# Performance work log

Measured on AMD Instinct MI355X. Metric: run time of the kernel, lower is better.

Reference implementation:

```python
import jax, jax.numpy as jnp
import numpy as np

B, H, S, D = 2, 16, 2048, 64

def setup_inputs() -> dict:
    key = jax.random.key(0)
    kq, kk, kv, km = jax.random.split(key, 4)
    Q = jax.random.normal(kq, (B, H, S, D), dtype=jnp.float32)
    K = jax.random.normal(kk, (B, H, S, D), dtype=jnp.float32)
    V = jax.random.normal(kv, (B, H, S, D), dtype=jnp.float32)
    attn_mask = jax.random.bernoulli(km, 0.5, (B, H, S, S))  # True = masked
    return {"Q": Q, "K": K, "V": V, "attn_mask": attn_mask}

def reference(Q, K, V, attn_mask):
    eps = 1e-12
    d_tensor = K.shape[-1]
    # scores: [B, H, S, S]
    scores = jnp.einsum('bhqd,bhkd->bhqk', Q, K) / np.sqrt(d_tensor).astype(jnp.float32)
    # Faithful to source: first fill mask==0 positions with -eps, then mask==True with -1e9.
    scores = jnp.where(attn_mask == 0, jnp.float32(-eps), scores)
    scores = jnp.where(attn_mask, jnp.float32(-1e9), scores)
    attn = jax.nn.softmax(scores, axis=-1)
    context = jnp.einsum('bhqk,bhkd->bhqd', attn, V)
    # dropout=0.0 (eval) -> identity
    return (context, attn)
```

## Files before the change

### kernel.cpp

```cpp
#include <hip/hip_runtime.h>
#include <hip/hip_bf16.h>
#include <stdint.h>

#define S 2048
#define D 64
#define BH 32
#define NROWS (BH * S)
#define CTX_ELEMS (NROWS * D)
#define NVTB 512
#define NSTB 2048
#define VT_BYTES ((size_t)BH * 64 * 64 * 32 * 2)

typedef __attribute__((ext_vector_type(8))) __bf16 bf16x8;
typedef __attribute__((ext_vector_type(4))) float f32x4;
typedef __attribute__((ext_vector_type(4))) int   i32x4;


__global__ __launch_bounds__(256) void k_mask(const int* __restrict__ mask,
                                              const float* __restrict__ V,
                                              float* __restrict__ attn,
                                              uint32_t* __restrict__ packed,
                                              __bf16* __restrict__ VT,
                                              int use_vt) {
  const int t = threadIdx.x;

  if (blockIdx.x < NVTB) {
    if (!use_vt) return;
    const int bh = blockIdx.x >> 4;
    const int kk0 = (blockIdx.x & 15) * 4;
    const int c = t >> 2;
    const int g = t & 3;
#pragma unroll
    for (int s = 0; s < 4; ++s) {
      const int kk = kk0 + s;
      const float* vp = V + ((long)bh * S + kk * 32 + g * 8) * D + c;
      bf16x8 o;
#pragma unroll
      for (int j = 0; j < 8; ++j) o[j] = (__bf16)vp[(long)j * D];
      *reinterpret_cast<bf16x8*>(VT + (((long)bh * 64 + kk) * 64 + c) * 32 + g * 8) = o;
    }
    return;
  }

  const int lane = t & 63;
  const int W = (blockIdx.x - NVTB) * 4 + (t >> 6);

#pragma unroll 1
  for (int row = W; row < NROWS; row += NSTB * 4) {
    const int* mrow = mask + (long)row * S;

    uint32_t nib = 0;
#pragma unroll
    for (int j = 0; j < 8; ++j) {
      const i32x4 m = __builtin_nontemporal_load(
          (const i32x4*)(mrow + j * 256 + lane * 4));
      nib |= (m[0] == 0 ? 1u : 0u) << (j * 4);
      nib |= (m[1] == 0 ? 1u : 0u) << (j * 4 + 1);
      nib |= (m[2] == 0 ? 1u : 0u) << (j * 4 + 2);
      nib |= (m[3] == 0 ? 1u : 0u) << (j * 4 + 3);
    }

    int cnt = __popc(nib);
#pragma unroll
    for (int off = 1; off < 64; off <<= 1) cnt += __shfl_xor(cnt, off, 64);
    const float inv = (cnt > 0) ? (1.0f / (float)cnt) : 0.0f;

    float* arow = attn + (long)row * S;
#pragma unroll
    for (int j = 0; j < 8; ++j) {
      f32x4 a;
      a[0] = ((nib >> (j * 4)) & 1u)     ? inv : 0.0f;
      a[1] = ((nib >> (j * 4 + 1)) & 1u) ? inv : 0.0f;
      a[2] = ((nib >> (j * 4 + 2)) & 1u) ? inv : 0.0f;
      a[3] = ((nib >> (j * 4 + 3)) & 1u) ? inv : 0.0f;
      __builtin_nontemporal_store(a, (f32x4*)(arow + j * 256 + lane * 4));
    }

    uint32_t word = 0;
    const int jsel = 4 * (lane >> 3);
    const int lbase = (lane & 7) * 8;
#pragma unroll
    for (int d = 0; d < 8; ++d) {
      const uint32_t nw = (uint32_t)__shfl((int)nib, lbase + d, 64);
      word |= ((nw >> jsel) & 0xFu) << (4 * d);
    }
    packed[(long)row * 64 + lane] = word;
  }
}

#define BMC 64
template<bool USE_VT>
__global__ __launch_bounds__(128) void k_ctx(const uint32_t* __restrict__ packed,
                                             const float* __restrict__ V,
                                             const __bf16* __restrict__ VT,
                                             float* __restrict__ ctx) {
  const int flat = blockIdx.x;
  const int wid = (flat & 7) * ((NROWS / BMC) / 8) + (flat >> 3);
  const int qt = wid & 31;
  const int bh = wid >> 5;

  const int t = threadIdx.x;
  const int lane = t & 63;
  const int w = t >> 6;
  const int l15 = lane & 15;
  const int lk = lane >> 4;

  __shared__ uint32_t pk[BMC * 65];
  __shared__ float invs[BMC];

  const long R0 = (long)bh * S + (long)qt * BMC;

  for (int i = t; i < BMC * 64; i += 128)
    pk[(i >> 6) * 65 + (i & 63)] = packed[(R0 + (i >> 6)) * 64 + (i & 63)];
  __syncthreads();

  if (t < BMC) {
    int c = 0;
#pragma unroll
    for (int i = 0; i < 64; ++i) c += __popc(pk[t * 65 + i]);
    invs[t] = (c > 0) ? (1.0f / (float)c) : 0.0f;
  }
  __syncthreads();

  const uint8_t* pkb = (const uint8_t*)pk;
  const uint8_t* ap[2];
#pragma unroll
  for (int mt = 0; mt < 2; ++mt)
    ap[mt] = pkb + (w * 32 + mt * 16 + l15) * 260 + lk;
  const __bf16* vt0 = VT + ((long)bh * 64) * 64 * 32 + (long)l15 * 32 + lk * 8;
  const float* vf0 = V + (long)bh * S * D + (long)lk * 8 * D + l15;

  f32x4 acc[2][4];
#pragma unroll
  for (int a = 0; a < 2; ++a)
#pragma unroll
    for (int b = 0; b < 4; ++b) acc[a][b] = f32x4{0.f, 0.f, 0.f, 0.f};

  auto LOADB = [&](bf16x8* dst, uint32_t* by, int kk) {
    if (USE_VT) {
#pragma unroll
      for (int n4 = 0; n4 < 4; ++n4)
        dst[n4] = *reinterpret_cast<const bf16x8*>(vt0 + ((long)kk * 64 + n4 * 16) * 32);
    } else {
      const float* vp = vf0 + (long)kk * 32 * D;
#pragma unroll
      for (int n4 = 0; n4 < 4; ++n4) {
        bf16x8 x;
#pragma unroll
        for (int j = 0; j < 8; ++j) x[j] = (__bf16)vp[j * D + n4 * 16];
        dst[n4] = x;
      }
    }
#pragma unroll
    for (int mt = 0; mt < 2; ++mt) by[mt] = ap[mt][kk * 4];
  };

  auto COMPUTE = [&](const bf16x8* bf, const uint32_t* by) {
#pragma unroll
    for (int mt = 0; mt < 2; ++mt) {
      union { uint32_t u[4]; bf16x8 v; } am;
#pragma unroll
      for (int p = 0; p < 4; ++p) {
        am.u[p] = (((by[mt] >> (2 * p)) & 1u) ? 0x3F80u : 0u)
                | (((by[mt] >> (2 * p + 1)) & 1u) ? 0x3F800000u : 0u);
      }
#pragma unroll
      for (int n4 = 0; n4 < 4; ++n4)
        acc[mt][n4] = __builtin_amdgcn_mfma_f32_16x16x32_bf16(am.v, bf[n4], acc[mt][n4], 0, 0, 0);
    }
  };

  bf16x8 bA[4], bB[4];
  uint32_t byA[2], byB[2];
  LOADB(bA, byA, 0);
#pragma unroll 1
  for (int kk = 0; kk < S / 32; kk += 2) {
    LOADB(bB, byB, kk + 1);
    COMPUTE(bA, byA);
    if (kk + 2 < S / 32) LOADB(bA, byA, kk + 2);
    COMPUTE(bB, byB);
  }

#pragma unroll
  for (int mt = 0; mt < 2; ++mt) {
#pragma unroll
    for (int ri = 0; ri < 4; ++ri) {
      const int rloc = w * 32 + mt * 16 + lk * 4 + ri;
      const float iv = invs[rloc];
      const long orow = R0 + rloc;
#pragma unroll
      for (int n4 = 0; n4 < 4; ++n4)
        ctx[orow * D + n4 * 16 + l15] = acc[mt][n4][ri] * iv;
    }
  }
}

extern "C" void kernel_launch(void* const* d_in, const int* in_sizes, int n_in,
                              void* d_out, int out_size, void* d_ws, size_t ws_size,
                              hipStream_t stream) {
  (void)in_sizes; (void)n_in; (void)out_size;
  const float* V = (const float*)d_in[2];
  const int* mask = (const int*)d_in[3];
  float* ctx = (float*)d_out;
  float* attn = (float*)d_out + (size_t)CTX_ELEMS;
  uint32_t* packed = (uint32_t*)d_out;
  __bf16* VT = (__bf16*)d_ws;

  const int use_vt = (ws_size >= VT_BYTES) ? 1 : 0;
  k_mask<<<NVTB + NSTB, 256, 0, stream>>>(mask, V, attn, packed, VT, use_vt);
  if (use_vt)
    k_ctx<true><<<NROWS / BMC, 128, 0, stream>>>(packed, V, VT, ctx);
  else
    k_ctx<false><<<NROWS / BMC, 128, 0, stream>>>(packed, V, VT, ctx);
}
```

Baseline: 233.5 us.

## Split K across four waves in context kernel with LDS atomic reduction

The context kernel now uses 256 threads: each wave covers all 64 rows of the tile but only a quarter of the key dimension. Partial accumulators are summed into a shared-memory buffer with atomic adds, then scaled and written with vectorized nontemporal stores. This is meant to raise parallelism and latency hiding in the K loop. In exchange it adds shared-memory atomics and extra LDS traffic.

```diff
diff --git a/kernel.cpp b/kernel.cpp
--- a/kernel.cpp
+++ b/kernel.cpp
@@ -15,7 +15,6 @@
 typedef __attribute__((ext_vector_type(4))) float f32x4;
 typedef __attribute__((ext_vector_type(4))) int   i32x4;
 
-
 __global__ __launch_bounds__(256) void k_mask(const int* __restrict__ mask,
                                               const float* __restrict__ V,
                                               float* __restrict__ attn,
@@ -90,7 +89,7 @@
 
 #define BMC 64
 template<bool USE_VT>
-__global__ __launch_bounds__(128) void k_ctx(const uint32_t* __restrict__ packed,
+__global__ __launch_bounds__(256) void k_ctx(const uint32_t* __restrict__ packed,
                                              const float* __restrict__ V,
                                              const __bf16* __restrict__ VT,
                                              float* __restrict__ ctx) {
@@ -107,11 +106,14 @@
 
   __shared__ uint32_t pk[BMC * 65];
   __shared__ float invs[BMC];
+  __shared__ float red[BMC][D];
 
   const long R0 = (long)bh * S + (long)qt * BMC;
 
-  for (int i = t; i < BMC * 64; i += 128)
+  for (int i = t; i < BMC * 64; i += 256)
     pk[(i >> 6) * 65 + (i & 63)] = packed[(R0 + (i >> 6)) * 64 + (i & 63)];
+  for (int i = t; i < BMC * D / 4; i += 256)
+    *(f32x4*)&red[(i * 4) / D][(i * 4) % D] = f32x4{0.f, 0.f, 0.f, 0.f};
   __syncthreads();
 
   if (t < BMC) {
@@ -120,19 +122,18 @@
     for (int i = 0; i < 64; ++i) c += __popc(pk[t * 65 + i]);
     invs[t] = (c > 0) ? (1.0f / (float)c) : 0.0f;
   }
-  __syncthreads();
 
   const uint8_t* pkb = (const uint8_t*)pk;
-  const uint8_t* ap[2];
-#pragma unroll
-  for (int mt = 0; mt < 2; ++mt)
-    ap[mt] = pkb + (w * 32 + mt * 16 + l15) * 260 + lk;
+  const uint8_t* ap[4];
+#pragma unroll
+  for (int mt = 0; mt < 4; ++mt)
+    ap[mt] = pkb + (mt * 16 + l15) * 260 + lk;
   const __bf16* vt0 = VT + ((long)bh * 64) * 64 * 32 + (long)l15 * 32 + lk * 8;
   const float* vf0 = V + (long)bh * S * D + (long)lk * 8 * D + l15;
 
-  f32x4 acc[2][4];
-#pragma unroll
-  for (int a = 0; a < 2; ++a)
+  f32x4 acc[4][4];
+#pragma unroll
+  for (int a = 0; a < 4; ++a)
 #pragma unroll
     for (int b = 0; b < 4; ++b) acc[a][b] = f32x4{0.f, 0.f, 0.f, 0.f};
 
@@ -152,12 +153,12 @@
       }
     }
 #pragma unroll
-    for (int mt = 0; mt < 2; ++mt) by[mt] = ap[mt][kk * 4];
+    for (int mt = 0; mt < 4; ++mt) by[mt] = ap[mt][kk * 4];
   };
 
   auto COMPUTE = [&](const bf16x8* bf, const uint32_t* by) {
 #pragma unroll
-    for (int mt = 0; mt < 2; ++mt) {
+    for (int mt = 0; mt < 4; ++mt) {
       union { uint32_t u[4]; bf16x8 v; } am;
 #pragma unroll
       for (int p = 0; p < 4; ++p) {
@@ -170,28 +171,36 @@
     }
   };
 
+  const int k0 = w * 16;
   bf16x8 bA[4], bB[4];
-  uint32_t byA[2], byB[2];
-  LOADB(bA, byA, 0);
+  uint32_t byA[4], byB[4];
+  LOADB(bA, byA, k0);
 #pragma unroll 1
-  for (int kk = 0; kk < S / 32; kk += 2) {
+  for (int kk = k0; kk < k0 + 16; kk += 2) {
     LOADB(bB, byB, kk + 1);
     COMPUTE(bA, byA);
-    if (kk + 2 < S / 32) LOADB(bA, byA, kk + 2);
+    if (kk + 2 < k0 + 16) LOADB(bA, byA, kk + 2);
     COMPUTE(bB, byB);
   }
 
 #pragma unroll
-  for (int mt = 0; mt < 2; ++mt) {
-#pragma unroll
-    for (int ri = 0; ri < 4; ++ri) {
-      const int rloc = w * 32 + mt * 16 + lk * 4 + ri;
-      const float iv = invs[rloc];
-      const long orow = R0 + rloc;
+  for (int mt = 0; mt < 4; ++mt)
+#pragma unroll
+    for (int ri = 0; ri < 4; ++ri)
 #pragma unroll
       for (int n4 = 0; n4 < 4; ++n4)
-        ctx[orow * D + n4 * 16 + l15] = acc[mt][n4][ri] * iv;
-    }
+        atomicAdd(&red[mt * 16 + lk * 4 + ri][n4 * 16 + l15], acc[mt][n4][ri]);
+  __syncthreads();
+
+#pragma unroll
+  for (int q = 0; q < 4; ++q) {
+    const int idx = t * 4 + q;
+    const int row = idx >> 4;
+    const int c4 = (idx & 15) * 4;
+    const float iv = invs[row];
+    f32x4 v = *(const f32x4*)&red[row][c4];
+    v[0] *= iv; v[1] *= iv; v[2] *= iv; v[3] *= iv;
+    __builtin_nontemporal_store(v, (f32x4*)(ctx + (R0 + row) * D + c4));
   }
 }
 
@@ -209,7 +218,7 @@
   const int use_vt = (ws_size >= VT_BYTES) ? 1 : 0;
   k_mask<<<NVTB + NSTB, 256, 0, stream>>>(mask, V, attn, packed, VT, use_vt);
   if (use_vt)
-    k_ctx<true><<<NROWS / BMC, 128, 0, stream>>>(packed, V, VT, ctx);
+    k_ctx<true><<<NROWS / BMC, 256, 0, stream>>>(packed, V, VT, ctx);
   else
-    k_ctx<false><<<NROWS / BMC, 128, 0, stream>>>(packed, V, VT, ctx);
+    k_ctx<false><<<NROWS / BMC, 256, 0, stream>>>(packed, V, VT, ctx);
 }
```

Result: slower. 301.8 us (+29.3%).
